# Kernel tuning notes

Measured on AMD Instinct MI355X. Metric: run time of the kernel, lower is better.

Reference implementation:

```python
import jax, jax.numpy as jnp
import numpy as np

N_NODES = 50000
D_IN = 128
HIDDEN = 128
UNITS_DENSE = 256
N_EDGES = 600000
N_PRED = 200000
N_SEL = 300000


def setup_inputs() -> dict:
    key = jax.random.key(0)
    ks = jax.random.split(key, 12)
    node_state = jax.random.normal(ks[0], (N_NODES, D_IN), jnp.float32)
    edge_index = jax.random.randint(ks[1], (2, N_EDGES), 0, N_NODES, jnp.int32)
    out_edges = jax.random.randint(ks[2], (2, N_PRED), 0, N_NODES, jnp.int32)
    set_idx = jnp.sort(jax.random.randint(ks[3], (N_SEL,), 0, 2 * N_PRED, jnp.int32))
    # Glorot-ish scaled weights
    W1 = jax.random.normal(ks[4], (D_IN, HIDDEN), jnp.float32) / np.float32(np.sqrt(D_IN))
    b1 = jnp.zeros((HIDDEN,), jnp.float32)
    W2 = jax.random.normal(ks[5], (HIDDEN, HIDDEN), jnp.float32) / np.float32(np.sqrt(HIDDEN))
    b2 = jnp.zeros((HIDDEN,), jnp.float32)
    dense_W = jax.random.normal(ks[6], (2 * 0 + HIDDEN, UNITS_DENSE), jnp.float32) / np.float32(np.sqrt(HIDDEN))
    dense_b = jnp.zeros((UNITS_DENSE,), jnp.float32)
    out_W = jax.random.normal(ks[7], (UNITS_DENSE, 2), jnp.float32) / np.float32(np.sqrt(UNITS_DENSE))
    out_b = jnp.zeros((2,), jnp.float32)
    return {
        "node_state": node_state, "edge_index": edge_index, "out_edges": out_edges,
        "set_idx": set_idx, "W1": W1, "b1": b1, "W2": W2, "b2": b2,
        "dense_W": dense_W, "dense_b": dense_b, "out_W": out_W, "out_b": out_b,
    }


def _graph_conv(h, src, dst, W, b):
    """DGL GraphConv, norm='both', no activation: D_in^{-1/2} A D_out^{-1/2} H W + b."""
    n = h.shape[0]
    ones = jnp.ones(src.shape[0], h.dtype)
    deg_out = jnp.clip(jax.ops.segment_sum(ones, src, num_segments=n), 1.0)  # [N]
    deg_in = jnp.clip(jax.ops.segment_sum(ones, dst, num_segments=n), 1.0)   # [N]
    h = (h * jax.lax.rsqrt(deg_out)[:, None]) @ W                            # [N, H]
    agg = jax.ops.segment_sum(h[src], dst, num_segments=n)                   # [N, H]
    return agg * jax.lax.rsqrt(deg_in)[:, None] + b


def reference(node_state, edge_index, out_edges, set_idx,
              W1, b1, W2, b2, dense_W, dense_b, out_W, out_b):
    src, dst = edge_index[0], edge_index[1]
    h = _graph_conv(node_state, src, dst, W1, b1)
    h = _graph_conv(h, src, dst, W2, b2)
    # concat along axis=0 as in the original: [2*E_pred, H]
    edge_state = jnp.concatenate([h[out_edges[0]], h[out_edges[1]]], axis=0)
    # boolean_mask replaced by equivalent gather of selected (True) rows
    edge_state_set = edge_state[set_idx]                                      # [N_SEL, H]
    hidden = jax.nn.relu(edge_state_set @ dense_W + dense_b)
    return jax.nn.softmax(hidden @ out_W + out_b, axis=-1)
```

## Files before the change

### kernel.cpp

```cpp
#include <hip/hip_runtime.h>

#define NN 50000
#define DD 128
#define NE 600000
#define NP 200000
#define NS 300000
#define NU 256
#define NBH 128
#define EPB 4688
#define NW 12500
#define NB64 782
#define NSCAN 49

typedef __attribute__((ext_vector_type(8))) short short8;
typedef __attribute__((ext_vector_type(4))) float floatx4;

__device__ inline float bf2f(unsigned int u16) {
    unsigned int x = u16 << 16;
    float f; __builtin_memcpy(&f, &x, 4); return f;
}
__device__ inline unsigned short f2bf(float f) {
    unsigned int x; __builtin_memcpy(&x, &f, 4);
    unsigned int lsb = (x >> 16) & 1u;
    x += 0x7fffu + lsb;
    return (unsigned short)(x >> 16);
}

__global__ __launch_bounds__(512) void k_hist(const int* __restrict__ ei,
                                              unsigned int* __restrict__ P,
                                              unsigned long long* __restrict__ status,
                                              const float* __restrict__ W1,
                                              const float* __restrict__ W2,
                                              const float* __restrict__ dW,
                                              unsigned short* __restrict__ BT1,
                                              unsigned short* __restrict__ BT2,
                                              unsigned short* __restrict__ BTd) {
    __shared__ unsigned int hw[NW];
    int b = blockIdx.x, half = blockIdx.y, tid = threadIdx.x;
    if (b == 0 && half == 0 && tid < 64) status[tid] = 0ull;
    for (int w = tid; w < NW; w += 512) hw[w] = 0;
    {
        int gid = (half * NBH + b) * 512 + tid;
        if (gid < 16384) { int rr = gid >> 7, cc = gid & 127; BT1[cc * 128 + rr] = f2bf(W1[gid]); }
        else if (gid < 32768) { int t2 = gid - 16384; int rr = t2 >> 7, cc = t2 & 127; BT2[cc * 128 + rr] = f2bf(W2[t2]); }
        else if (gid < 65536) { int t2 = gid - 32768; int rr = t2 >> 8, cc = t2 & 255; BTd[cc * 128 + rr] = f2bf(dW[t2]); }
    }
    __syncthreads();
    const int* src = ei + (size_t)half * NE;
    int e0 = b * EPB, e1 = min(e0 + EPB, NE);
    for (int e = e0 + tid; e < e1; e += 512) {
        int s = src[e];
        atomicAdd(&hw[s >> 2], 1u << ((s & 3) * 8));
    }
    __syncthreads();
    unsigned int* Pb = P + ((size_t)half * NBH + b) * NW;
    for (int w = tid; w < NW; w += 512) Pb[w] = hw[w];
}

__global__ __launch_bounds__(256) void k_mid(
    const unsigned int* __restrict__ P_hist, float* __restrict__ r,
    int* __restrict__ row_ptr, unsigned char* __restrict__ baseb,
    unsigned long long* __restrict__ status)
{
    int b = blockIdx.x, tid = threadIdx.x, lane = tid & 63, w = tid >> 6;
    int gid = b * 256 + tid;

    int4 v = {0, 0, 0, 0};
    if (gid < NW) {
        const unsigned int* Ph = P_hist + (size_t)NBH * NW + gid;
        int c0 = 0, c1 = 0, c2 = 0, c3 = 0;
        for (int b2 = 0; b2 < NBH; ++b2) {
            unsigned int x = Ph[(size_t)b2 * NW];
            c0 += x & 0xff; c1 += (x >> 8) & 0xff; c2 += (x >> 16) & 0xff; c3 += x >> 24;
        }
        v = (int4){c0, c1, c2, c3};
        float4 rr = {rsqrtf((float)max(c0, 1)), rsqrtf((float)max(c1, 1)),
                     rsqrtf((float)max(c2, 1)), rsqrtf((float)max(c3, 1))};
        *(float4*)(r + NN + gid * 4) = rr;
    } else if (gid < 2 * NW) {
        int wl = gid - NW;
        const unsigned int* Ph = P_hist + wl;
        int c0 = 0, c1 = 0, c2 = 0, c3 = 0;
        for (int b2 = 0; b2 < NBH; ++b2) {
            unsigned int x = Ph[(size_t)b2 * NW];
            c0 += x & 0xff; c1 += (x >> 8) & 0xff; c2 += (x >> 16) & 0xff; c3 += x >> 24;
        }
        float4 rr = {rsqrtf((float)max(c0, 1)), rsqrtf((float)max(c1, 1)),
                     rsqrtf((float)max(c2, 1)), rsqrtf((float)max(c3, 1))};
        *(float4*)(r + wl * 4) = rr;
    }

    if (b < NSCAN) {
        __shared__ int wsum[4];
        __shared__ long long sbase;
        int tot = v.x + v.y + v.z + v.w;
        int x = tot;
#pragma unroll
        for (int off = 1; off < 64; off <<= 1) {
            int y = __shfl_up(x, off);
            if (lane >= off) x += y;
        }
        if (lane == 63) wsum[w] = x;
        __syncthreads();
        int woff = 0;
#pragma unroll
        for (int i = 0; i < 4; ++i) if (i < w) woff += wsum[i];
        if (w == 0) {
            int btot = wsum[0] + wsum[1] + wsum[2] + wsum[3];
            if (lane == 0) {
                __threadfence();
                atomicExch(&status[b], (1ull << 62) | (unsigned long long)btot);
            }
            long long run = 0;
            if (lane < b) {
                unsigned long long s;
                do { s = atomicAdd(&status[lane], 0ull); } while (s == 0ull);
                run = (long long)(s & 0x3fffffffffffffffull);
            }
#pragma unroll
            for (int off = 32; off > 0; off >>= 1) run += __shfl_down(run, off);
            if (lane == 0) sbase = run;
        }
        __syncthreads();
        if (gid < NW) {
            int base = (int)sbase + woff + (x - tot);
            int4 o = {base, base + v.x, base + v.x + v.y, base + v.x + v.y + v.z};
            *(int4*)(row_ptr + gid * 4) = o;
        }
        if (b == 0 && tid == 0) row_ptr[NN] = NE;
    }

    int cb = b - NSCAN;
    if (cb >= 0 && cb < 196) {
        int n = cb * 256 + tid;
        if (n < NN) {
            int wl = n >> 2, sh = (n & 3) * 8;
            int run = 0;
            const unsigned int* Pd = P_hist + (size_t)NBH * NW;
            for (int b2 = 0; b2 < NBH; ++b2) {
                baseb[(size_t)b2 * NN + n] = (unsigned char)run;
                run += (Pd[(size_t)b2 * NW + wl] >> sh) & 0xff;
            }
        }
    }
}

__global__ __launch_bounds__(256) void k_gemm1_bucket(
    const float* __restrict__ A, const float* __restrict__ rs,
    const unsigned short* __restrict__ BT, unsigned short* __restrict__ Cm,
    const int* __restrict__ ei, const int* __restrict__ row_ptr,
    const unsigned char* __restrict__ baseb, int* __restrict__ col)
{
    __shared__ unsigned short sm[26112];
    int b = blockIdx.x, tid = threadIdx.x;

    if (b < NBH) {
        unsigned int* cw = (unsigned int*)sm;
        for (int w = tid; w < NW; w += 256) cw[w] = 0;
        __syncthreads();
        const unsigned char* bt = baseb + (size_t)b * NN;
        int e0 = b * EPB, e1 = min(e0 + EPB, NE);
        for (int e = e0 + tid; e < e1; e += 256) {
            int s = ei[e], d = ei[NE + e];
            int sh = (d & 3) * 8;
            unsigned int old = atomicAdd(&cw[d >> 2], 1u << sh);
            col[row_ptr[d] + (int)bt[d] + ((old >> sh) & 0xff)] = s;
        }
        return;
    }

    unsigned short (*As)[136] = (unsigned short(*)[136])sm;
    unsigned short (*Bs)[136] = (unsigned short(*)[136])(sm + 64 * 136);
    int lane = tid & 63, wave = tid >> 6;
    int quad = lane >> 4, l16 = lane & 15;
    int row0 = (b - NBH) * 64;

#pragma unroll
    for (int p = 0; p < 8; ++p) {
        int fid = tid + p * 256;
        int r = fid >> 5, c = fid & 31;
        int gr = row0 + r; if (gr > NN - 1) gr = NN - 1;
        float4 v = *(const float4*)(A + (size_t)gr * DD + c * 4);
        ushort4 u;
        u.x = f2bf(v.x); u.y = f2bf(v.y); u.z = f2bf(v.z); u.w = f2bf(v.w);
        *(ushort4*)&As[r][c * 4] = u;
    }
#pragma unroll
    for (int p = 0; p < 8; ++p) {
        int fid = tid + p * 256;
        int r = fid >> 4, c = fid & 15;
        *(uint4*)&Bs[r][c * 8] = *(const uint4*)(BT + (size_t)r * DD + c * 8);
    }
    __syncthreads();

    short8 af[4];
#pragma unroll
    for (int ks = 0; ks < 4; ++ks)
        af[ks] = *(const short8*)&As[wave * 16 + l16][ks * 32 + quad * 8];
    floatx4 acc[8];
#pragma unroll
    for (int nt = 0; nt < 8; ++nt) acc[nt] = (floatx4){0.f, 0.f, 0.f, 0.f};
#pragma unroll
    for (int ks = 0; ks < 4; ++ks) {
#pragma unroll
        for (int nt = 0; nt < 8; ++nt) {
            short8 bf = *(const short8*)&Bs[nt * 16 + l16][ks * 32 + quad * 8];
            acc[nt] = __builtin_amdgcn_mfma_f32_16x16x32_bf16(af[ks], bf, acc[nt], 0, 0, 0);
        }
    }
    int rbase = row0 + wave * 16 + quad * 4;
#pragma unroll
    for (int r = 0; r < 4; ++r) {
        int gr = rbase + r;
        if (gr < NN) {
            float s = rs[gr];
#pragma unroll
            for (int nt = 0; nt < 8; ++nt)
                Cm[(size_t)gr * DD + nt * 16 + l16] = f2bf(acc[nt][r] * s);
        }
    }
}

__global__ __launch_bounds__(256) void k_gemm_bf(const unsigned short* __restrict__ A,
                                                 const float* __restrict__ rs,
                                                 const unsigned short* __restrict__ BT,
                                                 unsigned short* __restrict__ Cm) {
    __shared__ unsigned short As[64][136];
    __shared__ unsigned short Bs[128][136];
    int tid = threadIdx.x, lane = tid & 63, wave = tid >> 6;
    int quad = lane >> 4, l16 = lane & 15;
    int row0 = blockIdx.x * 64;

#pragma unroll
    for (int p = 0; p < 4; ++p) {
        int fid = tid + p * 256;
        int r = fid >> 4, c = fid & 15;
        int gr = row0 + r; if (gr > NN - 1) gr = NN - 1;
        *(uint4*)&As[r][c * 8] = *(const uint4*)(A + (size_t)gr * DD + c * 8);
    }
#pragma unroll
    for (int p = 0; p < 8; ++p) {
        int fid = tid + p * 256;
        int r = fid >> 4, c = fid & 15;
        *(uint4*)&Bs[r][c * 8] = *(const uint4*)(BT + (size_t)r * DD + c * 8);
    }
    __syncthreads();

    short8 af[4];
#pragma unroll
    for (int ks = 0; ks < 4; ++ks)
        af[ks] = *(const short8*)&As[wave * 16 + l16][ks * 32 + quad * 8];
    floatx4 acc[8];
#pragma unroll
    for (int nt = 0; nt < 8; ++nt) acc[nt] = (floatx4){0.f, 0.f, 0.f, 0.f};
#pragma unroll
    for (int ks = 0; ks < 4; ++ks) {
#pragma unroll
        for (int nt = 0; nt < 8; ++nt) {
            short8 bf = *(const short8*)&Bs[nt * 16 + l16][ks * 32 + quad * 8];
            acc[nt] = __builtin_amdgcn_mfma_f32_16x16x32_bf16(af[ks], bf, acc[nt], 0, 0, 0);
        }
    }
    int rbase = row0 + wave * 16 + quad * 4;
#pragma unroll
    for (int r = 0; r < 4; ++r) {
        int gr = rbase + r;
        if (gr < NN) {
            float s = rs[gr];
#pragma unroll
            for (int nt = 0; nt < 8; ++nt)
                Cm[(size_t)gr * DD + nt * 16 + l16] = f2bf(acc[nt][r] * s);
        }
    }
}

__global__ __launch_bounds__(256) void k_aggregate(const unsigned short* __restrict__ T,
                                                   const int* __restrict__ row_ptr,
                                                   const int* __restrict__ col,
                                                   const float* __restrict__ r_in,
                                                   const float* __restrict__ b,
                                                   unsigned short* __restrict__ H) {
    int wave = threadIdx.x >> 6, lane = threadIdx.x & 63;
    int sub = lane >> 4, l16 = lane & 15;
    int node = blockIdx.x * 16 + wave * 4 + sub;
    if (node >= NN) return;
    int beg = row_ptr[node], end = row_ptr[node + 1];
    float a0 = 0.f, a1 = 0.f, a2 = 0.f, a3 = 0.f, a4 = 0.f, a5 = 0.f, a6 = 0.f, a7 = 0.f;
    for (int base = beg; base < end; base += 16) {
        int m = end - base; if (m > 16) m = 16;
        int myidx = (l16 < m) ? col[base + l16] : 0;
        int j = 0;
        for (; j + 4 <= m; j += 4) {
            int s0 = __shfl(myidx, (sub << 4) | j);
            int s1 = __shfl(myidx, (sub << 4) | (j + 1));
            int s2 = __shfl(myidx, (sub << 4) | (j + 2));
            int s3 = __shfl(myidx, (sub << 4) | (j + 3));
            uint4 v0 = *(const uint4*)(T + (size_t)s0 * DD + l16 * 8);
            uint4 v1 = *(const uint4*)(T + (size_t)s1 * DD + l16 * 8);
            uint4 v2 = *(const uint4*)(T + (size_t)s2 * DD + l16 * 8);
            uint4 v3 = *(const uint4*)(T + (size_t)s3 * DD + l16 * 8);
            a0 += bf2f(v0.x & 0xffff) + bf2f(v1.x & 0xffff) + bf2f(v2.x & 0xffff) + bf2f(v3.x & 0xffff);
            a1 += bf2f(v0.x >> 16)    + bf2f(v1.x >> 16)    + bf2f(v2.x >> 16)    + bf2f(v3.x >> 16);
            a2 += bf2f(v0.y & 0xffff) + bf2f(v1.y & 0xffff) + bf2f(v2.y & 0xffff) + bf2f(v3.y & 0xffff);
            a3 += bf2f(v0.y >> 16)    + bf2f(v1.y >> 16)    + bf2f(v2.y >> 16)    + bf2f(v3.y >> 16);
            a4 += bf2f(v0.z & 0xffff) + bf2f(v1.z & 0xffff) + bf2f(v2.z & 0xffff) + bf2f(v3.z & 0xffff);
            a5 += bf2f(v0.z >> 16)    + bf2f(v1.z >> 16)    + bf2f(v2.z >> 16)    + bf2f(v3.z >> 16);
            a6 += bf2f(v0.w & 0xffff) + bf2f(v1.w & 0xffff) + bf2f(v2.w & 0xffff) + bf2f(v3.w & 0xffff);
            a7 += bf2f(v0.w >> 16)    + bf2f(v1.w >> 16)    + bf2f(v2.w >> 16)    + bf2f(v3.w >> 16);
        }
        for (; j < m; ++j) {
            int s0 = __shfl(myidx, (sub << 4) | j);
            uint4 v0 = *(const uint4*)(T + (size_t)s0 * DD + l16 * 8);
            a0 += bf2f(v0.x & 0xffff); a1 += bf2f(v0.x >> 16);
            a2 += bf2f(v0.y & 0xffff); a3 += bf2f(v0.y >> 16);
            a4 += bf2f(v0.z & 0xffff); a5 += bf2f(v0.z >> 16);
            a6 += bf2f(v0.w & 0xffff); a7 += bf2f(v0.w >> 16);
        }
    }
    float rv = r_in[node];
    float4 bl = *(const float4*)(b + l16 * 8);
    float4 bh = *(const float4*)(b + l16 * 8 + 4);
    uint4 w;
    w.x = (unsigned int)f2bf(a0 * rv + bl.x) | ((unsigned int)f2bf(a1 * rv + bl.y) << 16);
    w.y = (unsigned int)f2bf(a2 * rv + bl.z) | ((unsigned int)f2bf(a3 * rv + bl.w) << 16);
    w.z = (unsigned int)f2bf(a4 * rv + bh.x) | ((unsigned int)f2bf(a5 * rv + bh.y) << 16);
    w.w = (unsigned int)f2bf(a6 * rv + bh.z) | ((unsigned int)f2bf(a7 * rv + bh.w) << 16);
    *(uint4*)(H + (size_t)node * DD + l16 * 8) = w;
}

__global__ __launch_bounds__(256) void k_mlp_mfma(const unsigned short* __restrict__ H2,
                                                  const unsigned short* __restrict__ BTd,
                                                  const float* __restrict__ db,
                                                  const float* __restrict__ oW,
                                                  const float* __restrict__ ob,
                                                  float* __restrict__ P) {
    __shared__ unsigned short As[64][136];
    __shared__ unsigned short Bs[128][136];
    int tid = threadIdx.x, lane = tid & 63, wave = tid >> 6;
    int quad = lane >> 4, l16 = lane & 15;
    int row0 = blockIdx.x * 64;
#pragma unroll
    for (int p = 0; p < 4; ++p) {
        int fid = tid + p * 256;
        int r = fid >> 4, c = fid & 15;
        int gr = row0 + r; if (gr > NN - 1) gr = NN - 1;
        *(uint4*)&As[r][c * 8] = *(const uint4*)(H2 + (size_t)gr * DD + c * 8);
    }
    short8 af[4];
    floatx4 acc[16];
#pragma unroll
    for (int i = 0; i < 16; ++i) acc[i] = (floatx4){0.f, 0.f, 0.f, 0.f};

    for (int ch = 0; ch < 2; ++ch) {
        __syncthreads();
#pragma unroll
        for (int p = 0; p < 8; ++p) {
            int fid = tid + p * 256;
            int r = fid >> 4, c = fid & 15;
            *(uint4*)&Bs[r][c * 8] = *(const uint4*)(BTd + (size_t)(ch * 128 + r) * DD + c * 8);
        }
        __syncthreads();
        if (ch == 0) {
#pragma unroll
            for (int ks = 0; ks < 4; ++ks)
                af[ks] = *(const short8*)&As[wave * 16 + l16][ks * 32 + quad * 8];
        }
#pragma unroll
        for (int ks = 0; ks < 4; ++ks) {
#pragma unroll
            for (int nt = 0; nt < 8; ++nt) {
                short8 bf = *(const short8*)&Bs[nt * 16 + l16][ks * 32 + quad * 8];
                acc[ch * 8 + nt] =
                    __builtin_amdgcn_mfma_f32_16x16x32_bf16(af[ks], bf, acc[ch * 8 + nt], 0, 0, 0);
            }
        }
    }
    int rbase = row0 + wave * 16 + quad * 4;
#pragma unroll
    for (int r = 0; r < 4; ++r) {
        float p0 = 0.f, p1 = 0.f;
#pragma unroll
        for (int ch = 0; ch < 2; ++ch) {
#pragma unroll
            for (int nt = 0; nt < 8; ++nt) {
                int colc = ch * 128 + nt * 16 + l16;
                float h = acc[ch * 8 + nt][r] + db[colc];
                h = fmaxf(h, 0.f);
                p0 += h * oW[2 * colc];
                p1 += h * oW[2 * colc + 1];
            }
        }
#pragma unroll
        for (int m = 8; m >= 1; m >>= 1) {
            p0 += __shfl_xor(p0, m, 16);
            p1 += __shfl_xor(p1, m, 16);
        }
        if (l16 == 0) {
            int gr = rbase + r;
            if (gr < NN) {
                float l0 = p0 + ob[0], l1 = p1 + ob[1];
                float mx = fmaxf(l0, l1);
                float e0 = __expf(l0 - mx), e1 = __expf(l1 - mx);
                float inv = 1.f / (e0 + e1);
                float2 pr = {e0 * inv, e1 * inv};
                *(float2*)(P + 2 * gr) = pr;
            }
        }
    }
}

__global__ void k_gather(const int* __restrict__ sidx, const int* __restrict__ oe,
                         const float* __restrict__ P, float* __restrict__ out) {
    int i = blockIdx.x * 256 + threadIdx.x;
    if (i >= NS) return;
    int node = oe[sidx[i]];
    float2 v = *(const float2*)(P + 2 * node);
    *(float2*)(out + 2 * i) = v;
}

extern "C" void kernel_launch(void* const* d_in, const int* in_sizes, int n_in,
                              void* d_out, int out_size, void* d_ws, size_t ws_size,
                              hipStream_t stream) {
    const float* node_state = (const float*)d_in[0];
    const int* ei   = (const int*)d_in[1];
    const int* oe   = (const int*)d_in[2];
    const int* sidx = (const int*)d_in[3];
    const float* W1 = (const float*)d_in[4];
    const float* b1 = (const float*)d_in[5];
    const float* W2 = (const float*)d_in[6];
    const float* b2 = (const float*)d_in[7];
    const float* dW = (const float*)d_in[8];
    const float* db = (const float*)d_in[9];
    const float* oW = (const float*)d_in[10];
    const float* ob = (const float*)d_in[11];
    float* out = (float*)d_out;

    char* ws = (char*)d_ws;
    size_t off = 0;
    auto carve = [&](size_t bytes) -> char* {
        char* p = ws + off;
        off = (off + bytes + 255) & ~(size_t)255;
        return p;
    };
    float* r       = (float*)carve((size_t)2 * NN * 4);
    int*   row_ptr = (int*)carve((size_t)(NN + 1) * 4);
    int*   col     = (int*)carve((size_t)NE * 4);
    unsigned int* P_hist = (unsigned int*)carve((size_t)2 * NBH * NW * 4);
    unsigned char* baseb = (unsigned char*)carve((size_t)NBH * NN);
    unsigned long long* status = (unsigned long long*)carve(64 * 8);
    unsigned short* t   = (unsigned short*)carve((size_t)NN * DD * 2);
    unsigned short* h   = (unsigned short*)carve((size_t)NN * DD * 2);
    unsigned short* BT1 = (unsigned short*)carve((size_t)DD * DD * 2);
    unsigned short* BT2 = (unsigned short*)carve((size_t)DD * DD * 2);
    unsigned short* BTd = (unsigned short*)carve((size_t)DD * NU * 2);
    float* P = (float*)t;

    float* r_out = r;
    float* r_in  = r + NN;

    k_hist<<<dim3(NBH, 2), 512, 0, stream>>>(ei, P_hist, status, W1, W2, dW,
                                             BT1, BT2, BTd);
    k_mid<<<245, 256, 0, stream>>>(P_hist, r, row_ptr, baseb, status);

    k_gemm1_bucket<<<NBH + NB64, 256, 0, stream>>>(node_state, r_out, BT1, t,
                                                   ei, row_ptr, baseb, col);
    k_aggregate<<<(NN + 15) / 16, 256, 0, stream>>>(t, row_ptr, col, r_in, b1, h);

    k_gemm_bf<<<NB64, 256, 0, stream>>>(h, r_out, BT2, t);
    k_aggregate<<<(NN + 15) / 16, 256, 0, stream>>>(t, row_ptr, col, r_in, b2, h);

    k_mlp_mfma<<<NB64, 256, 0, stream>>>(h, BTd, db, oW, ob, P);
    k_gather<<<(NS + 255) / 256, 256, 0, stream>>>(sidx, oe, P, out);
}
```

Baseline: 230.8 us.

## Replace deterministic per-block histogram CSR build with global atomics and unroll aggregate

The degree counting and CSR construction no longer use per-block shared-memory histograms with a deterministic per-block base offset table. They now use global atomicAdd on degree counters, a scan kernel that also seeds a cursor array, and atomic cursor increments for scattering column indices. This drops the large P_hist and baseb buffers and their 128-deep serial loops, but adds many contended global atomics and makes the neighbor order within each row nondeterministic. The aggregation loop is also fully unrolled to 16 gathers per chunk with masked weights, which raises memory-level parallelism at the cost of wasted loads on short rows.

```diff
diff --git a/kernel.cpp b/kernel.cpp
--- a/kernel.cpp
+++ b/kernel.cpp
@@ -6,11 +6,11 @@
 #define NP 200000
 #define NS 300000
 #define NU 256
-#define NBH 128
-#define EPB 4688
 #define NW 12500
 #define NB64 782
 #define NSCAN 49
+#define BBK 256
+#define EPB2 2344
 
 typedef __attribute__((ext_vector_type(8))) short short8;
 typedef __attribute__((ext_vector_type(4))) float floatx4;
@@ -26,145 +26,110 @@
     return (unsigned short)(x >> 16);
 }
 
-__global__ __launch_bounds__(512) void k_hist(const int* __restrict__ ei,
-                                              unsigned int* __restrict__ P,
-                                              unsigned long long* __restrict__ status,
-                                              const float* __restrict__ W1,
-                                              const float* __restrict__ W2,
-                                              const float* __restrict__ dW,
-                                              unsigned short* __restrict__ BT1,
-                                              unsigned short* __restrict__ BT2,
-                                              unsigned short* __restrict__ BTd) {
-    __shared__ unsigned int hw[NW];
-    int b = blockIdx.x, half = blockIdx.y, tid = threadIdx.x;
-    if (b == 0 && half == 0 && tid < 64) status[tid] = 0ull;
-    for (int w = tid; w < NW; w += 512) hw[w] = 0;
-    {
-        int gid = (half * NBH + b) * 512 + tid;
-        if (gid < 16384) { int rr = gid >> 7, cc = gid & 127; BT1[cc * 128 + rr] = f2bf(W1[gid]); }
-        else if (gid < 32768) { int t2 = gid - 16384; int rr = t2 >> 7, cc = t2 & 127; BT2[cc * 128 + rr] = f2bf(W2[t2]); }
-        else if (gid < 65536) { int t2 = gid - 32768; int rr = t2 >> 8, cc = t2 & 255; BTd[cc * 128 + rr] = f2bf(dW[t2]); }
-    }
-    __syncthreads();
-    const int* src = ei + (size_t)half * NE;
-    int e0 = b * EPB, e1 = min(e0 + EPB, NE);
-    for (int e = e0 + tid; e < e1; e += 512) {
-        int s = src[e];
-        atomicAdd(&hw[s >> 2], 1u << ((s & 3) * 8));
-    }
-    __syncthreads();
-    unsigned int* Pb = P + ((size_t)half * NBH + b) * NW;
-    for (int w = tid; w < NW; w += 512) Pb[w] = hw[w];
-}
-
-__global__ __launch_bounds__(256) void k_mid(
-    const unsigned int* __restrict__ P_hist, float* __restrict__ r,
-    int* __restrict__ row_ptr, unsigned char* __restrict__ baseb,
-    unsigned long long* __restrict__ status)
+__global__ __launch_bounds__(256) void k_prep(int* __restrict__ deg,
+                                              unsigned long long* __restrict__ status) {
+    int gid = blockIdx.x * 256 + threadIdx.x;
+    if (gid < 64) status[gid] = 0ull;
+    if (gid < 2 * NW) ((int4*)deg)[gid] = (int4){0, 0, 0, 0};
+}
+
+__global__ __launch_bounds__(256) void k_deg(const int* __restrict__ ei,
+                                             int* __restrict__ deg) {
+    int nt = gridDim.x * 256;
+    for (int w = blockIdx.x * 256 + threadIdx.x; w < 2 * NE / 4; w += nt) {
+        int4 e = ((const int4*)ei)[w];
+        int base = (w >= NE / 4) ? NN : 0;
+        atomicAdd(&deg[base + e.x], 1);
+        atomicAdd(&deg[base + e.y], 1);
+        atomicAdd(&deg[base + e.z], 1);
+        atomicAdd(&deg[base + e.w], 1);
+    }
+}
+
+__global__ __launch_bounds__(256) void k_scan(
+    const int* __restrict__ deg, float* __restrict__ r,
+    int* __restrict__ row_ptr, int* __restrict__ cur,
+    unsigned long long* __restrict__ status,
+    const float* __restrict__ W1, const float* __restrict__ W2,
+    const float* __restrict__ dW,
+    unsigned short* __restrict__ BT1, unsigned short* __restrict__ BT2,
+    unsigned short* __restrict__ BTd)
 {
     int b = blockIdx.x, tid = threadIdx.x, lane = tid & 63, w = tid >> 6;
     int gid = b * 256 + tid;
 
     int4 v = {0, 0, 0, 0};
     if (gid < NW) {
-        const unsigned int* Ph = P_hist + (size_t)NBH * NW + gid;
-        int c0 = 0, c1 = 0, c2 = 0, c3 = 0;
-        for (int b2 = 0; b2 < NBH; ++b2) {
-            unsigned int x = Ph[(size_t)b2 * NW];
-            c0 += x & 0xff; c1 += (x >> 8) & 0xff; c2 += (x >> 16) & 0xff; c3 += x >> 24;
-        }
-        v = (int4){c0, c1, c2, c3};
-        float4 rr = {rsqrtf((float)max(c0, 1)), rsqrtf((float)max(c1, 1)),
-                     rsqrtf((float)max(c2, 1)), rsqrtf((float)max(c3, 1))};
-        *(float4*)(r + NN + gid * 4) = rr;
-    } else if (gid < 2 * NW) {
-        int wl = gid - NW;
-        const unsigned int* Ph = P_hist + wl;
-        int c0 = 0, c1 = 0, c2 = 0, c3 = 0;
-        for (int b2 = 0; b2 < NBH; ++b2) {
-            unsigned int x = Ph[(size_t)b2 * NW];
-            c0 += x & 0xff; c1 += (x >> 8) & 0xff; c2 += (x >> 16) & 0xff; c3 += x >> 24;
-        }
-        float4 rr = {rsqrtf((float)max(c0, 1)), rsqrtf((float)max(c1, 1)),
-                     rsqrtf((float)max(c2, 1)), rsqrtf((float)max(c3, 1))};
-        *(float4*)(r + wl * 4) = rr;
-    }
-
-    if (b < NSCAN) {
-        __shared__ int wsum[4];
-        __shared__ long long sbase;
-        int tot = v.x + v.y + v.z + v.w;
-        int x = tot;
-#pragma unroll
-        for (int off = 1; off < 64; off <<= 1) {
-            int y = __shfl_up(x, off);
-            if (lane >= off) x += y;
-        }
-        if (lane == 63) wsum[w] = x;
-        __syncthreads();
-        int woff = 0;
-#pragma unroll
-        for (int i = 0; i < 4; ++i) if (i < w) woff += wsum[i];
-        if (w == 0) {
-            int btot = wsum[0] + wsum[1] + wsum[2] + wsum[3];
-            if (lane == 0) {
-                __threadfence();
-                atomicExch(&status[b], (1ull << 62) | (unsigned long long)btot);
-            }
-            long long run = 0;
-            if (lane < b) {
-                unsigned long long s;
-                do { s = atomicAdd(&status[lane], 0ull); } while (s == 0ull);
-                run = (long long)(s & 0x3fffffffffffffffull);
-            }
-#pragma unroll
-            for (int off = 32; off > 0; off >>= 1) run += __shfl_down(run, off);
-            if (lane == 0) sbase = run;
-        }
-        __syncthreads();
-        if (gid < NW) {
-            int base = (int)sbase + woff + (x - tot);
-            int4 o = {base, base + v.x, base + v.x + v.y, base + v.x + v.y + v.z};
-            *(int4*)(row_ptr + gid * 4) = o;
-        }
-        if (b == 0 && tid == 0) row_ptr[NN] = NE;
-    }
-
-    int cb = b - NSCAN;
-    if (cb >= 0 && cb < 196) {
-        int n = cb * 256 + tid;
-        if (n < NN) {
-            int wl = n >> 2, sh = (n & 3) * 8;
-            int run = 0;
-            const unsigned int* Pd = P_hist + (size_t)NBH * NW;
-            for (int b2 = 0; b2 < NBH; ++b2) {
-                baseb[(size_t)b2 * NN + n] = (unsigned char)run;
-                run += (Pd[(size_t)b2 * NW + wl] >> sh) & 0xff;
-            }
-        }
-    }
+        int4 din  = ((const int4*)(deg + NN))[gid];
+        int4 dout = ((const int4*)deg)[gid];
+        v = din;
+        float4 ri = {rsqrtf((float)max(din.x, 1)),  rsqrtf((float)max(din.y, 1)),
+                     rsqrtf((float)max(din.z, 1)),  rsqrtf((float)max(din.w, 1))};
+        float4 ro = {rsqrtf((float)max(dout.x, 1)), rsqrtf((float)max(dout.y, 1)),
+                     rsqrtf((float)max(dout.z, 1)), rsqrtf((float)max(dout.w, 1))};
+        *(float4*)(r + NN + gid * 4) = ri;
+        *(float4*)(r + gid * 4) = ro;
+    }
+
+    __shared__ int wsum[4];
+    __shared__ long long sbase;
+    int tot = v.x + v.y + v.z + v.w;
+    int x = tot;
+#pragma unroll
+    for (int off = 1; off < 64; off <<= 1) {
+        int y = __shfl_up(x, off);
+        if (lane >= off) x += y;
+    }
+    if (lane == 63) wsum[w] = x;
+    __syncthreads();
+    int woff = 0;
+#pragma unroll
+    for (int i = 0; i < 4; ++i) if (i < w) woff += wsum[i];
+    if (w == 0) {
+        int btot = wsum[0] + wsum[1] + wsum[2] + wsum[3];
+        if (lane == 0) {
+            __threadfence();
+            atomicExch(&status[b], (1ull << 62) | (unsigned long long)btot);
+        }
+        long long run = 0;
+        if (lane < b) {
+            unsigned long long s;
+            do { s = atomicAdd(&status[lane], 0ull); } while (s == 0ull);
+            run = (long long)(s & 0x3fffffffffffffffull);
+        }
+#pragma unroll
+        for (int off = 32; off > 0; off >>= 1) run += __shfl_down(run, off);
+        if (lane == 0) sbase = run;
+    }
+    for (int t = gid; t < 65536; t += NSCAN * 256) {
+        if (t < 16384) { int rr = t >> 7, cc = t & 127; BT1[cc * 128 + rr] = f2bf(W1[t]); }
+        else if (t < 32768) { int t2 = t - 16384; int rr = t2 >> 7, cc = t2 & 127; BT2[cc * 128 + rr] = f2bf(W2[t2]); }
+        else { int t2 = t - 32768; int rr = t2 >> 8, cc = t2 & 255; BTd[cc * 128 + rr] = f2bf(dW[t2]); }
+    }
+    __syncthreads();
+    if (gid < NW) {
+        int base = (int)sbase + woff + (x - tot);
+        int4 o = {base, base + v.x, base + v.x + v.y, base + v.x + v.y + v.z};
+        ((int4*)row_ptr)[gid] = o;
+        ((int4*)cur)[gid] = o;
+    }
+    if (b == 0 && tid == 0) row_ptr[NN] = NE;
 }
 
 __global__ __launch_bounds__(256) void k_gemm1_bucket(
     const float* __restrict__ A, const float* __restrict__ rs,
     const unsigned short* __restrict__ BT, unsigned short* __restrict__ Cm,
-    const int* __restrict__ ei, const int* __restrict__ row_ptr,
-    const unsigned char* __restrict__ baseb, int* __restrict__ col)
+    const int* __restrict__ ei, int* __restrict__ cur, int* __restrict__ col)
 {
     __shared__ unsigned short sm[26112];
     int b = blockIdx.x, tid = threadIdx.x;
 
-    if (b < NBH) {
-        unsigned int* cw = (unsigned int*)sm;
-        for (int w = tid; w < NW; w += 256) cw[w] = 0;
-        __syncthreads();
-        const unsigned char* bt = baseb + (size_t)b * NN;
-        int e0 = b * EPB, e1 = min(e0 + EPB, NE);
+    if (b < BBK) {
+        int e0 = b * EPB2, e1 = min(e0 + EPB2, NE);
         for (int e = e0 + tid; e < e1; e += 256) {
             int s = ei[e], d = ei[NE + e];
-            int sh = (d & 3) * 8;
-            unsigned int old = atomicAdd(&cw[d >> 2], 1u << sh);
-            col[row_ptr[d] + (int)bt[d] + ((old >> sh) & 0xff)] = s;
+            int pos = atomicAdd(&cur[d], 1);
+            col[pos] = s;
         }
         return;
     }
@@ -173,23 +138,23 @@
     unsigned short (*Bs)[136] = (unsigned short(*)[136])(sm + 64 * 136);
     int lane = tid & 63, wave = tid >> 6;
     int quad = lane >> 4, l16 = lane & 15;
-    int row0 = (b - NBH) * 64;
+    int row0 = (b - BBK) * 64;
 
 #pragma unroll
     for (int p = 0; p < 8; ++p) {
         int fid = tid + p * 256;
-        int r = fid >> 5, c = fid & 31;
-        int gr = row0 + r; if (gr > NN - 1) gr = NN - 1;
+        int rr = fid >> 5, c = fid & 31;
+        int gr = row0 + rr; if (gr > NN - 1) gr = NN - 1;
         float4 v = *(const float4*)(A + (size_t)gr * DD + c * 4);
         ushort4 u;
         u.x = f2bf(v.x); u.y = f2bf(v.y); u.z = f2bf(v.z); u.w = f2bf(v.w);
-        *(ushort4*)&As[r][c * 4] = u;
+        *(ushort4*)&As[rr][c * 4] = u;
     }
 #pragma unroll
     for (int p = 0; p < 8; ++p) {
         int fid = tid + p * 256;
-        int r = fid >> 4, c = fid & 15;
-        *(uint4*)&Bs[r][c * 8] = *(const uint4*)(BT + (size_t)r * DD + c * 8);
+        int rr = fid >> 4, c = fid & 15;
+        *(uint4*)&Bs[rr][c * 8] = *(const uint4*)(BT + (size_t)rr * DD + c * 8);
     }
     __syncthreads();
 
@@ -210,13 +175,13 @@
     }
     int rbase = row0 + wave * 16 + quad * 4;
 #pragma unroll
-    for (int r = 0; r < 4; ++r) {
-        int gr = rbase + r;
+    for (int rr = 0; rr < 4; ++rr) {
+        int gr = rbase + rr;
         if (gr < NN) {
             float s = rs[gr];
 #pragma unroll
             for (int nt = 0; nt < 8; ++nt)
-                Cm[(size_t)gr * DD + nt * 16 + l16] = f2bf(acc[nt][r] * s);
+                Cm[(size_t)gr * DD + nt * 16 + l16] = f2bf(acc[nt][rr] * s);
         }
     }
 }
@@ -234,15 +199,15 @@
 #pragma unroll
     for (int p = 0; p < 4; ++p) {
         int fid = tid + p * 256;
-        int r = fid >> 4, c = fid & 15;
-        int gr = row0 + r; if (gr > NN - 1) gr = NN - 1;
-        *(uint4*)&As[r][c * 8] = *(const uint4*)(A + (size_t)gr * DD + c * 8);
+        int rr = fid >> 4, c = fid & 15;
+        int gr = row0 + rr; if (gr > NN - 1) gr = NN - 1;
+        *(uint4*)&As[rr][c * 8] = *(const uint4*)(A + (size_t)gr * DD + c * 8);
     }
 #pragma unroll
     for (int p = 0; p < 8; ++p) {
         int fid = tid + p * 256;
-        int r = fid >> 4, c = fid & 15;
-        *(uint4*)&Bs[r][c * 8] = *(const uint4*)(BT + (size_t)r * DD + c * 8);
+        int rr = fid >> 4, c = fid & 15;
+        *(uint4*)&Bs[rr][c * 8] = *(const uint4*)(BT + (size_t)rr * DD + c * 8);
     }
     __syncthreads();
 
@@ -263,16 +228,22 @@
     }
     int rbase = row0 + wave * 16 + quad * 4;
 #pragma unroll
-    for (int r = 0; r < 4; ++r) {
-        int gr = rbase + r;
+    for (int rr = 0; rr < 4; ++rr) {
+        int gr = rbase + rr;
         if (gr < NN) {
             float s = rs[gr];
 #pragma unroll
             for (int nt = 0; nt < 8; ++nt)
-                Cm[(size_t)gr * DD + nt * 16 + l16] = f2bf(acc[nt][r] * s);
-        }
-    }
-}
+                Cm[(size_t)gr * DD + nt * 16 + l16] = f2bf(acc[nt][rr] * s);
+        }
+    }
+}
+
+#define ACC8(u, wk) \
+    a0 += wk * bf2f(u.x & 0xffff); a1 += wk * bf2f(u.x >> 16); \
+    a2 += wk * bf2f(u.y & 0xffff); a3 += wk * bf2f(u.y >> 16); \
+    a4 += wk * bf2f(u.z & 0xffff); a5 += wk * bf2f(u.z >> 16); \
+    a6 += wk * bf2f(u.w & 0xffff); a7 += wk * bf2f(u.w >> 16);
 
 __global__ __launch_bounds__(256) void k_aggregate(const unsigned short* __restrict__ T,
                                                    const int* __restrict__ row_ptr,
@@ -286,36 +257,47 @@
     if (node >= NN) return;
     int beg = row_ptr[node], end = row_ptr[node + 1];
     float a0 = 0.f, a1 = 0.f, a2 = 0.f, a3 = 0.f, a4 = 0.f, a5 = 0.f, a6 = 0.f, a7 = 0.f;
+    const unsigned short* Tl = T + l16 * 8;
+    int grp = sub << 4;
     for (int base = beg; base < end; base += 16) {
         int m = end - base; if (m > 16) m = 16;
         int myidx = (l16 < m) ? col[base + l16] : 0;
-        int j = 0;
-        for (; j + 4 <= m; j += 4) {
-            int s0 = __shfl(myidx, (sub << 4) | j);
-            int s1 = __shfl(myidx, (sub << 4) | (j + 1));
-            int s2 = __shfl(myidx, (sub << 4) | (j + 2));
-            int s3 = __shfl(myidx, (sub << 4) | (j + 3));
-            uint4 v0 = *(const uint4*)(T + (size_t)s0 * DD + l16 * 8);
-            uint4 v1 = *(const uint4*)(T + (size_t)s1 * DD + l16 * 8);
-            uint4 v2 = *(const uint4*)(T + (size_t)s2 * DD + l16 * 8);
-            uint4 v3 = *(const uint4*)(T + (size_t)s3 * DD + l16 * 8);
-            a0 += bf2f(v0.x & 0xffff) + bf2f(v1.x & 0xffff) + bf2f(v2.x & 0xffff) + bf2f(v3.x & 0xffff);
-            a1 += bf2f(v0.x >> 16)    + bf2f(v1.x >> 16)    + bf2f(v2.x >> 16)    + bf2f(v3.x >> 16);
-            a2 += bf2f(v0.y & 0xffff) + bf2f(v1.y & 0xffff) + bf2f(v2.y & 0xffff) + bf2f(v3.y & 0xffff);
-            a3 += bf2f(v0.y >> 16)    + bf2f(v1.y >> 16)    + bf2f(v2.y >> 16)    + bf2f(v3.y >> 16);
-            a4 += bf2f(v0.z & 0xffff) + bf2f(v1.z & 0xffff) + bf2f(v2.z & 0xffff) + bf2f(v3.z & 0xffff);
-            a5 += bf2f(v0.z >> 16)    + bf2f(v1.z >> 16)    + bf2f(v2.z >> 16)    + bf2f(v3.z >> 16);
-            a6 += bf2f(v0.w & 0xffff) + bf2f(v1.w & 0xffff) + bf2f(v2.w & 0xffff) + bf2f(v3.w & 0xffff);
-            a7 += bf2f(v0.w >> 16)    + bf2f(v1.w >> 16)    + bf2f(v2.w >> 16)    + bf2f(v3.w >> 16);
-        }
-        for (; j < m; ++j) {
-            int s0 = __shfl(myidx, (sub << 4) | j);
-            uint4 v0 = *(const uint4*)(T + (size_t)s0 * DD + l16 * 8);
-            a0 += bf2f(v0.x & 0xffff); a1 += bf2f(v0.x >> 16);
-            a2 += bf2f(v0.y & 0xffff); a3 += bf2f(v0.y >> 16);
-            a4 += bf2f(v0.z & 0xffff); a5 += bf2f(v0.z >> 16);
-            a6 += bf2f(v0.w & 0xffff); a7 += bf2f(v0.w >> 16);
-        }
+        int s0  = __shfl(myidx, grp | 0),  s1  = __shfl(myidx, grp | 1);
+        int s2  = __shfl(myidx, grp | 2),  s3  = __shfl(myidx, grp | 3);
+        int s4  = __shfl(myidx, grp | 4),  s5  = __shfl(myidx, grp | 5);
+        int s6  = __shfl(myidx, grp | 6),  s7  = __shfl(myidx, grp | 7);
+        int s8  = __shfl(myidx, grp | 8),  s9  = __shfl(myidx, grp | 9);
+        int s10 = __shfl(myidx, grp | 10), s11 = __shfl(myidx, grp | 11);
+        int s12 = __shfl(myidx, grp | 12), s13 = __shfl(myidx, grp | 13);
+        int s14 = __shfl(myidx, grp | 14), s15 = __shfl(myidx, grp | 15);
+        uint4 u0  = *(const uint4*)(Tl + (size_t)s0  * DD);
+        uint4 u1  = *(const uint4*)(Tl + (size_t)s1  * DD);
+        uint4 u2  = *(const uint4*)(Tl + (size_t)s2  * DD);
+        uint4 u3  = *(const uint4*)(Tl + (size_t)s3  * DD);
+        uint4 u4  = *(const uint4*)(Tl + (size_t)s4  * DD);
+        uint4 u5  = *(const uint4*)(Tl + (size_t)s5  * DD);
+        uint4 u6  = *(const uint4*)(Tl + (size_t)s6  * DD);
+        uint4 u7  = *(const uint4*)(Tl + (size_t)s7  * DD);
+        uint4 u8  = *(const uint4*)(Tl + (size_t)s8  * DD);
+        uint4 u9  = *(const uint4*)(Tl + (size_t)s9  * DD);
+        uint4 u10 = *(const uint4*)(Tl + (size_t)s10 * DD);
+        uint4 u11 = *(const uint4*)(Tl + (size_t)s11 * DD);
+        uint4 u12 = *(const uint4*)(Tl + (size_t)s12 * DD);
+        uint4 u13 = *(const uint4*)(Tl + (size_t)s13 * DD);
+        uint4 u14 = *(const uint4*)(Tl + (size_t)s14 * DD);
+        uint4 u15 = *(const uint4*)(Tl + (size_t)s15 * DD);
+        float w0  = 0  < m ? 1.f : 0.f, w1  = 1  < m ? 1.f : 0.f;
+        float w2  = 2  < m ? 1.f : 0.f, w3  = 3  < m ? 1.f : 0.f;
+        float w4  = 4  < m ? 1.f : 0.f, w5  = 5  < m ? 1.f : 0.f;
+        float w6  = 6  < m ? 1.f : 0.f, w7  = 7  < m ? 1.f : 0.f;
+        float w8  = 8  < m ? 1.f : 0.f, w9  = 9  < m ? 1.f : 0.f;
+        float w10 = 10 < m ? 1.f : 0.f, w11 = 11 < m ? 1.f : 0.f;
+        float w12 = 12 < m ? 1.f : 0.f, w13 = 13 < m ? 1.f : 0.f;
+        float w14 = 14 < m ? 1.f : 0.f, w15 = 15 < m ? 1.f : 0.f;
+        ACC8(u0, w0)   ACC8(u1, w1)   ACC8(u2, w2)   ACC8(u3, w3)
+        ACC8(u4, w4)   ACC8(u5, w5)   ACC8(u6, w6)   ACC8(u7, w7)
+        ACC8(u8, w8)   ACC8(u9, w9)   ACC8(u10, w10) ACC8(u11, w11)
+        ACC8(u12, w12) ACC8(u13, w13) ACC8(u14, w14) ACC8(u15, w15)
     }
     float rv = r_in[node];
     float4 bl = *(const float4*)(b + l16 * 8);
@@ -342,9 +324,9 @@
 #pragma unroll
     for (int p = 0; p < 4; ++p) {
         int fid = tid + p * 256;
-        int r = fid >> 4, c = fid & 15;
-        int gr = row0 + r; if (gr > NN - 1) gr = NN - 1;
-        *(uint4*)&As[r][c * 8] = *(const uint4*)(H2 + (size_t)gr * DD + c * 8);
+        int rr = fid >> 4, c = fid & 15;
+        int gr = row0 + rr; if (gr > NN - 1) gr = NN - 1;
+        *(uint4*)&As[rr][c * 8] = *(const uint4*)(H2 + (size_t)gr * DD + c * 8);
     }
     short8 af[4];
     floatx4 acc[16];
@@ -356,8 +338,8 @@
 #pragma unroll
         for (int p = 0; p < 8; ++p) {
             int fid = tid + p * 256;
-            int r = fid >> 4, c = fid & 15;
-            *(uint4*)&Bs[r][c * 8] = *(const uint4*)(BTd + (size_t)(ch * 128 + r) * DD + c * 8);
+            int rr = fid >> 4, c = fid & 15;
+            *(uint4*)&Bs[rr][c * 8] = *(const uint4*)(BTd + (size_t)(ch * 128 + rr) * DD + c * 8);
         }
         __syncthreads();
         if (ch == 0) {
@@ -377,14 +359,14 @@
     }
     int rbase = row0 + wave * 16 + quad * 4;
 #pragma unroll
-    for (int r = 0; r < 4; ++r) {
+    for (int rr = 0; rr < 4; ++rr) {
         float p0 = 0.f, p1 = 0.f;
 #pragma unroll
         for (int ch = 0; ch < 2; ++ch) {
 #pragma unroll
             for (int nt = 0; nt < 8; ++nt) {
                 int colc = ch * 128 + nt * 16 + l16;
-                float h = acc[ch * 8 + nt][r] + db[colc];
+                float h = acc[ch * 8 + nt][rr] + db[colc];
                 h = fmaxf(h, 0.f);
                 p0 += h * oW[2 * colc];
                 p1 += h * oW[2 * colc + 1];
@@ -396,7 +378,7 @@
             p1 += __shfl_xor(p1, m, 16);
         }
         if (l16 == 0) {
-            int gr = rbase + r;
+            int gr = rbase + rr;
             if (gr < NN) {
                 float l0 = p0 + ob[0], l1 = p1 + ob[1];
                 float mx = fmaxf(l0, l1);
@@ -444,9 +426,9 @@
     };
     float* r       = (float*)carve((size_t)2 * NN * 4);
     int*   row_ptr = (int*)carve((size_t)(NN + 1) * 4);
+    int*   cur     = (int*)carve((size_t)NN * 4);
     int*   col     = (int*)carve((size_t)NE * 4);
-    unsigned int* P_hist = (unsigned int*)carve((size_t)2 * NBH * NW * 4);
-    unsigned char* baseb = (unsigned char*)carve((size_t)NBH * NN);
+    int*   deg     = (int*)carve((size_t)2 * NN * 4);
     unsigned long long* status = (unsigned long long*)carve(64 * 8);
     unsigned short* t   = (unsigned short*)carve((size_t)NN * DD * 2);
     unsigned short* h   = (unsigned short*)carve((size_t)NN * DD * 2);
@@ -458,12 +440,13 @@
     float* r_out = r;
     float* r_in  = r + NN;
 
-    k_hist<<<dim3(NBH, 2), 512, 0, stream>>>(ei, P_hist, status, W1, W2, dW,
-                                             BT1, BT2, BTd);
-    k_mid<<<245, 256, 0, stream>>>(P_hist, r, row_ptr, baseb, status);
-
-    k_gemm1_bucket<<<NBH + NB64, 256, 0, stream>>>(node_state, r_out, BT1, t,
-                                                   ei, row_ptr, baseb, col);
+    k_prep<<<98, 256, 0, stream>>>(deg, status);
+    k_deg<<<1172, 256, 0, stream>>>(ei, deg);
+    k_scan<<<NSCAN, 256, 0, stream>>>(deg, r, row_ptr, cur, status,
+                                      W1, W2, dW, BT1, BT2, BTd);
+
+    k_gemm1_bucket<<<BBK + NB64, 256, 0, stream>>>(node_state, r_out, BT1, t,
+                                                   ei, cur, col);
     k_aggregate<<<(NN + 15) / 16, 256, 0, stream>>>(t, row_ptr, col, r_in, b1, h);
 
     k_gemm_bf<<<NB64, 256, 0, stream>>>(h, r_out, BT2, t);
```

Result: slower. 269.3 us (+16.7%).

## Halve histogram blocks and fuse bucket-base computation into degree scan

Applied to the files above, without the earlier changes.

Halves the number of histogram and bucketing blocks (NBH 128→64, edges per block doubled), which halves the per-block histogram storage and the reduction loops in k_mid. The per-bucket base-offset computation is folded into the degree-count loop of the scan blocks, so k_mid launches only two groups of 49 blocks and no longer has a separate pass over the histogram. k_aggregate also gets an occupancy hint in its launch bounds. The risks are lower parallelism in k_hist and bucketing, and per-block byte counters that must still fit in 8 bits with more edges per block.

```diff
diff --git a/kernel.cpp b/kernel.cpp
--- a/kernel.cpp
+++ b/kernel.cpp
@@ -6,8 +6,8 @@
 #define NP 200000
 #define NS 300000
 #define NU 256
-#define NBH 128
-#define EPB 4688
+#define NBH 64
+#define EPB 9375
 #define NW 12500
 #define NB64 782
 #define NSCAN 49
@@ -43,7 +43,7 @@
         int gid = (half * NBH + b) * 512 + tid;
         if (gid < 16384) { int rr = gid >> 7, cc = gid & 127; BT1[cc * 128 + rr] = f2bf(W1[gid]); }
         else if (gid < 32768) { int t2 = gid - 16384; int rr = t2 >> 7, cc = t2 & 127; BT2[cc * 128 + rr] = f2bf(W2[t2]); }
-        else if (gid < 65536) { int t2 = gid - 32768; int rr = t2 >> 8, cc = t2 & 255; BTd[cc * 128 + rr] = f2bf(dW[t2]); }
+        else { int t2 = gid - 32768; int rr = t2 >> 8, cc = t2 & 255; BTd[cc * 128 + rr] = f2bf(dW[t2]); }
     }
     __syncthreads();
     const int* src = ei + (size_t)half * NE;
@@ -63,34 +63,28 @@
     unsigned long long* __restrict__ status)
 {
     int b = blockIdx.x, tid = threadIdx.x, lane = tid & 63, w = tid >> 6;
-    int gid = b * 256 + tid;
-
-    int4 v = {0, 0, 0, 0};
-    if (gid < NW) {
-        const unsigned int* Ph = P_hist + (size_t)NBH * NW + gid;
-        int c0 = 0, c1 = 0, c2 = 0, c3 = 0;
-        for (int b2 = 0; b2 < NBH; ++b2) {
-            unsigned int x = Ph[(size_t)b2 * NW];
-            c0 += x & 0xff; c1 += (x >> 8) & 0xff; c2 += (x >> 16) & 0xff; c3 += x >> 24;
-        }
-        v = (int4){c0, c1, c2, c3};
-        float4 rr = {rsqrtf((float)max(c0, 1)), rsqrtf((float)max(c1, 1)),
-                     rsqrtf((float)max(c2, 1)), rsqrtf((float)max(c3, 1))};
-        *(float4*)(r + NN + gid * 4) = rr;
-    } else if (gid < 2 * NW) {
-        int wl = gid - NW;
-        const unsigned int* Ph = P_hist + wl;
-        int c0 = 0, c1 = 0, c2 = 0, c3 = 0;
-        for (int b2 = 0; b2 < NBH; ++b2) {
-            unsigned int x = Ph[(size_t)b2 * NW];
-            c0 += x & 0xff; c1 += (x >> 8) & 0xff; c2 += (x >> 16) & 0xff; c3 += x >> 24;
-        }
-        float4 rr = {rsqrtf((float)max(c0, 1)), rsqrtf((float)max(c1, 1)),
-                     rsqrtf((float)max(c2, 1)), rsqrtf((float)max(c3, 1))};
-        *(float4*)(r + wl * 4) = rr;
-    }
 
     if (b < NSCAN) {
+        int gid = b * 256 + tid;
+        int4 v = {0, 0, 0, 0};
+        if (gid < NW) {
+            const unsigned int* Ph = P_hist + (size_t)NBH * NW + gid;
+            int c0 = 0, c1 = 0, c2 = 0, c3 = 0;
+            unsigned char* bb = baseb + gid * 4;
+            for (int b2 = 0; b2 < NBH; ++b2) {
+                unsigned int x = Ph[(size_t)b2 * NW];
+                uchar4 pb = {(unsigned char)c0, (unsigned char)c1,
+                             (unsigned char)c2, (unsigned char)c3};
+                *(uchar4*)(bb + (size_t)b2 * NN) = pb;
+                c0 += x & 0xff; c1 += (x >> 8) & 0xff;
+                c2 += (x >> 16) & 0xff; c3 += x >> 24;
+            }
+            v = (int4){c0, c1, c2, c3};
+            float4 rr = {rsqrtf((float)max(c0, 1)), rsqrtf((float)max(c1, 1)),
+                         rsqrtf((float)max(c2, 1)), rsqrtf((float)max(c3, 1))};
+            *(float4*)(r + NN + gid * 4) = rr;
+        }
+
         __shared__ int wsum[4];
         __shared__ long long sbase;
         int tot = v.x + v.y + v.z + v.w;
@@ -128,19 +122,19 @@
             *(int4*)(row_ptr + gid * 4) = o;
         }
         if (b == 0 && tid == 0) row_ptr[NN] = NE;
-    }
-
-    int cb = b - NSCAN;
-    if (cb >= 0 && cb < 196) {
-        int n = cb * 256 + tid;
-        if (n < NN) {
-            int wl = n >> 2, sh = (n & 3) * 8;
-            int run = 0;
-            const unsigned int* Pd = P_hist + (size_t)NBH * NW;
+    } else {
+        int wl = (b - NSCAN) * 256 + tid;
+        if (wl < NW) {
+            const unsigned int* Ph = P_hist + wl;
+            int c0 = 0, c1 = 0, c2 = 0, c3 = 0;
             for (int b2 = 0; b2 < NBH; ++b2) {
-                baseb[(size_t)b2 * NN + n] = (unsigned char)run;
-                run += (Pd[(size_t)b2 * NW + wl] >> sh) & 0xff;
-            }
+                unsigned int x = Ph[(size_t)b2 * NW];
+                c0 += x & 0xff; c1 += (x >> 8) & 0xff;
+                c2 += (x >> 16) & 0xff; c3 += x >> 24;
+            }
+            float4 rr = {rsqrtf((float)max(c0, 1)), rsqrtf((float)max(c1, 1)),
+                         rsqrtf((float)max(c2, 1)), rsqrtf((float)max(c3, 1))};
+            *(float4*)(r + wl * 4) = rr;
         }
     }
 }
@@ -178,18 +172,18 @@
 #pragma unroll
     for (int p = 0; p < 8; ++p) {
         int fid = tid + p * 256;
-        int r = fid >> 5, c = fid & 31;
-        int gr = row0 + r; if (gr > NN - 1) gr = NN - 1;
+        int rr = fid >> 5, c = fid & 31;
+        int gr = row0 + rr; if (gr > NN - 1) gr = NN - 1;
         float4 v = *(const float4*)(A + (size_t)gr * DD + c * 4);
         ushort4 u;
         u.x = f2bf(v.x); u.y = f2bf(v.y); u.z = f2bf(v.z); u.w = f2bf(v.w);
-        *(ushort4*)&As[r][c * 4] = u;
+        *(ushort4*)&As[rr][c * 4] = u;
     }
 #pragma unroll
     for (int p = 0; p < 8; ++p) {
         int fid = tid + p * 256;
-        int r = fid >> 4, c = fid & 15;
-        *(uint4*)&Bs[r][c * 8] = *(const uint4*)(BT + (size_t)r * DD + c * 8);
+        int rr = fid >> 4, c = fid & 15;
+        *(uint4*)&Bs[rr][c * 8] = *(const uint4*)(BT + (size_t)rr * DD + c * 8);
     }
     __syncthreads();
 
@@ -210,13 +204,13 @@
     }
     int rbase = row0 + wave * 16 + quad * 4;
 #pragma unroll
-    for (int r = 0; r < 4; ++r) {
-        int gr = rbase + r;
+    for (int rr = 0; rr < 4; ++rr) {
+        int gr = rbase + rr;
         if (gr < NN) {
             float s = rs[gr];
 #pragma unroll
             for (int nt = 0; nt < 8; ++nt)
-                Cm[(size_t)gr * DD + nt * 16 + l16] = f2bf(acc[nt][r] * s);
+                Cm[(size_t)gr * DD + nt * 16 + l16] = f2bf(acc[nt][rr] * s);
         }
     }
 }
@@ -234,15 +228,15 @@
 #pragma unroll
     for (int p = 0; p < 4; ++p) {
         int fid = tid + p * 256;
-        int r = fid >> 4, c = fid & 15;
-        int gr = row0 + r; if (gr > NN - 1) gr = NN - 1;
-        *(uint4*)&As[r][c * 8] = *(const uint4*)(A + (size_t)gr * DD + c * 8);
+        int rr = fid >> 4, c = fid & 15;
+        int gr = row0 + rr; if (gr > NN - 1) gr = NN - 1;
+        *(uint4*)&As[rr][c * 8] = *(const uint4*)(A + (size_t)gr * DD + c * 8);
     }
 #pragma unroll
     for (int p = 0; p < 8; ++p) {
         int fid = tid + p * 256;
-        int r = fid >> 4, c = fid & 15;
-        *(uint4*)&Bs[r][c * 8] = *(const uint4*)(BT + (size_t)r * DD + c * 8);
+        int rr = fid >> 4, c = fid & 15;
+        *(uint4*)&Bs[rr][c * 8] = *(const uint4*)(BT + (size_t)rr * DD + c * 8);
     }
     __syncthreads();
 
@@ -263,23 +257,23 @@
     }
     int rbase = row0 + wave * 16 + quad * 4;
 #pragma unroll
-    for (int r = 0; r < 4; ++r) {
-        int gr = rbase + r;
+    for (int rr = 0; rr < 4; ++rr) {
+        int gr = rbase + rr;
         if (gr < NN) {
             float s = rs[gr];
 #pragma unroll
             for (int nt = 0; nt < 8; ++nt)
-                Cm[(size_t)gr * DD + nt * 16 + l16] = f2bf(acc[nt][r] * s);
-        }
-    }
-}
-
-__global__ __launch_bounds__(256) void k_aggregate(const unsigned short* __restrict__ T,
-                                                   const int* __restrict__ row_ptr,
-                                                   const int* __restrict__ col,
-                                                   const float* __restrict__ r_in,
-                                                   const float* __restrict__ b,
-                                                   unsigned short* __restrict__ H) {
+                Cm[(size_t)gr * DD + nt * 16 + l16] = f2bf(acc[nt][rr] * s);
+        }
+    }
+}
+
+__global__ __launch_bounds__(256, 6) void k_aggregate(const unsigned short* __restrict__ T,
+                                                      const int* __restrict__ row_ptr,
+                                                      const int* __restrict__ col,
+                                                      const float* __restrict__ r_in,
+                                                      const float* __restrict__ b,
+                                                      unsigned short* __restrict__ H) {
     int wave = threadIdx.x >> 6, lane = threadIdx.x & 63;
     int sub = lane >> 4, l16 = lane & 15;
     int node = blockIdx.x * 16 + wave * 4 + sub;
@@ -342,9 +336,9 @@
 #pragma unroll
     for (int p = 0; p < 4; ++p) {
         int fid = tid + p * 256;
-        int r = fid >> 4, c = fid & 15;
-        int gr = row0 + r; if (gr > NN - 1) gr = NN - 1;
-        *(uint4*)&As[r][c * 8] = *(const uint4*)(H2 + (size_t)gr * DD + c * 8);
+        int rr = fid >> 4, c = fid & 15;
+        int gr = row0 + rr; if (gr > NN - 1) gr = NN - 1;
+        *(uint4*)&As[rr][c * 8] = *(const uint4*)(H2 + (size_t)gr * DD + c * 8);
     }
     short8 af[4];
     floatx4 acc[16];
@@ -356,8 +350,8 @@
 #pragma unroll
         for (int p = 0; p < 8; ++p) {
             int fid = tid + p * 256;
-            int r = fid >> 4, c = fid & 15;
-            *(uint4*)&Bs[r][c * 8] = *(const uint4*)(BTd + (size_t)(ch * 128 + r) * DD + c * 8);
+            int rr = fid >> 4, c = fid & 15;
+            *(uint4*)&Bs[rr][c * 8] = *(const uint4*)(BTd + (size_t)(ch * 128 + rr) * DD + c * 8);
         }
         __syncthreads();
         if (ch == 0) {
@@ -377,14 +371,14 @@
     }
     int rbase = row0 + wave * 16 + quad * 4;
 #pragma unroll
-    for (int r = 0; r < 4; ++r) {
+    for (int rr = 0; rr < 4; ++rr) {
         float p0 = 0.f, p1 = 0.f;
 #pragma unroll
         for (int ch = 0; ch < 2; ++ch) {
 #pragma unroll
             for (int nt = 0; nt < 8; ++nt) {
                 int colc = ch * 128 + nt * 16 + l16;
-                float h = acc[ch * 8 + nt][r] + db[colc];
+                float h = acc[ch * 8 + nt][rr] + db[colc];
                 h = fmaxf(h, 0.f);
                 p0 += h * oW[2 * colc];
                 p1 += h * oW[2 * colc + 1];
@@ -396,7 +390,7 @@
             p1 += __shfl_xor(p1, m, 16);
         }
         if (l16 == 0) {
-            int gr = rbase + r;
+            int gr = rbase + rr;
             if (gr < NN) {
                 float l0 = p0 + ob[0], l1 = p1 + ob[1];
                 float mx = fmaxf(l0, l1);
@@ -460,7 +454,7 @@
 
     k_hist<<<dim3(NBH, 2), 512, 0, stream>>>(ei, P_hist, status, W1, W2, dW,
                                              BT1, BT2, BTd);
-    k_mid<<<245, 256, 0, stream>>>(P_hist, r, row_ptr, baseb, status);
+    k_mid<<<2 * NSCAN, 256, 0, stream>>>(P_hist, r, row_ptr, baseb, status);
 
     k_gemm1_bucket<<<NBH + NB64, 256, 0, stream>>>(node_state, r_out, BT1, t,
                                                    ei, row_ptr, baseb, col);
```

After: 230.4 us. About the same (-0.2%).
